# Performance work log

Hardware: AMD Instinct MI355X
Metric: run time of the kernel (lower is better)

The kernel has to match this reference:

```python
import jax, jax.numpy as jnp
import numpy as np

B, T, HOP = 4, 200, 120
N = T * HOP
M1, A1 = 40, 5            # mcep_order+1, apdc_order+1
HID, COND = 256, 192
SR = 24000.0
ALPHA = 0.466             # frequency-warping for 24 kHz
PD = 4                    # Pade order
PADE = jnp.asarray([1.0, 0.4999273, 0.1067005, 0.00956526, 0.0003041358], jnp.float32)
SIGN = jnp.asarray([1.0, -1.0, 1.0, -1.0], jnp.float32)  # + for odd Pade tap index
F0_MEAN, F0_STD = 5.0, 0.25
MCEP_MEAN, MCEP_STD = 0.0, 1.0
APDC_MEAN, APDC_STD = 0.0, 1.0
NOISE_RATIO, SP_RATE, F0_RATE = 0.5, 1.0, 1.0


def mc2b(mc, a):
    """SPTK mc2b: mel-cepstrum -> MLSA filter coefficients (scan over order)."""
    mc_rev = jnp.moveaxis(mc, -1, 0)[::-1]  # [M1, B, T]
    def step(carry, c):
        b = c - a * carry
        return b, b
    _, bs = jax.lax.scan(step, jnp.zeros_like(mc_rev[0]), mc_rev)
    return jnp.moveaxis(bs[::-1], 0, -1)


def _mlsafir(x, b, d):
    # SPTK mlsafir, vectorized over the PD Pade taps.
    # x: [PD], b: [M1], d: [PD, M1+1]
    aa = 1.0 - ALPHA * ALPHA
    d1 = aa * x + ALPHA * d[:, 1]
    def step(prev, di):  # d_new[i] = d[i] + a*(d[i+1] - d_new[i-1]) : order recurrence
        d_i, d_ip1 = di
        new = d_i + ALPHA * (d_ip1 - prev)
        return new, new
    xs = (d[:, 2:M1].T, d[:, 3:M1 + 1].T)  # [M1-2, PD]
    _, dupd = jax.lax.scan(step, d1, xs)    # [M1-2, PD]
    y = jnp.einsum('mp,m->p', dupd, b[2:])
    # delay-line shift: new d = [x, d1, d1, dupd[2..M]]
    new_d = jnp.concatenate([x[:, None], d1[:, None], d1[:, None], dupd.T], axis=1)
    return y, new_d


def _mlsa_step(state, inp):
    d1a, d1b, d2, pt2 = state
    x, b = inp
    x = x * jnp.exp(b[0])           # gain
    # ---- stage 1 (uses b[1] only), SPTK mlsadf1 ----
    aa = 1.0 - ALPHA * ALPHA
    na = aa * d1b[:PD] + ALPHA * d1a[1:]
    npt = na * b[1]
    v1 = npt * PADE[1:]
    x1 = x + jnp.sum(v1 * SIGN)
    y1 = jnp.sum(v1) + x1
    d1a = jnp.concatenate([d1a[:1], na])
    d1b = jnp.concatenate([x1[None], npt])
    # ---- stage 2 (orders >= 2), SPTK mlsadf2 ----
    fy, d2 = _mlsafir(pt2[:PD], b, d2)
    v2 = fy * PADE[1:]
    x2 = y1 + jnp.sum(v2 * SIGN)
    y2 = jnp.sum(v2) + x2
    pt2 = jnp.concatenate([x2[None], fy])
    return (d1a, d1b, d2, pt2), y2


def mlsa_filter(exc, b_up):
    # exc: [N], b_up: [N, M1] -> filtered waveform [N]
    init = (jnp.zeros(PD + 1, jnp.float32), jnp.zeros(PD + 1, jnp.float32),
            jnp.zeros((PD, M1 + 1), jnp.float32), jnp.zeros(PD + 1, jnp.float32))
    _, y = jax.lax.scan(_mlsa_step, init, (exc, b_up))
    return y


def _forward(mceps, apdcs, frame_f0s, noise,
             Wm, bm, Wa, ba, Wf, bf, Wpa, bpa, Wpp, bpp,
             Wrp, brp, Wra, bra, Wap):
    # linear feature embed + sum
    hs = mceps @ Wm + bm + apdcs @ Wa + ba + frame_f0s @ Wf + bf   # [B,T,HID]
    ca = hs @ Wpa + bpa                                             # prenet_a cond [B,T,COND]
    cp = hs @ Wpp + bpp                                             # prenet_p cond
    # denorm (+ exp for log-f0)
    f0 = jnp.exp(frame_f0s[..., 0] * F0_STD + F0_MEAN) * F0_RATE    # [B,T]
    sp = mceps * MCEP_STD + MCEP_MEAN
    ap = apdcs * APDC_STD + APDC_MEAN
    # per-path mel-cepstra with prenet residuals
    mc_p = sp * SP_RATE + 0.1 * jnp.tanh(cp @ Wrp + brp)
    mc_a = sp * SP_RATE + 0.1 * jnp.tanh(ca @ Wra + bra) + ap @ Wap
    b_p = mc2b(mc_p, ALPHA)
    b_a = mc2b(mc_a, ALPHA)
    # excitation at sample rate
    f0_up = jnp.repeat(f0, HOP, axis=1)                             # [B,N]
    phase = jnp.cumsum(f0_up / SR, axis=1)
    w = jnp.floor(phase)
    wprev = jnp.concatenate([jnp.zeros_like(w[:, :1]), w[:, :-1]], axis=1)
    amp = jnp.sqrt(SR / jnp.maximum(f0_up, 1.0))
    pulse = jnp.where(w > wprev, amp, 0.0)
    exc_p = pulse * (1.0 - NOISE_RATIO)
    exc_a = noise * NOISE_RATIO
    # run both (periodic/aperiodic) MLSA synthesis filters in one batched scan
    excs = jnp.concatenate([exc_p, exc_a], axis=0)                  # [2B,N]
    bs = jnp.repeat(jnp.concatenate([b_p, b_a], axis=0), HOP, axis=1)  # [2B,N,M1]
    wavs = jax.vmap(mlsa_filter)(excs, bs)                          # [2B,N]
    return wavs[:B] + wavs[B:]


_forward_jit = jax.jit(_forward)


def setup_inputs() -> dict:
    key = jax.random.key(0)
    ks = jax.random.split(key, 20)
    decay = 0.3 / (1.0 + jnp.arange(M1, dtype=jnp.float32))  # realistic cepstral decay (filter stability)
    return {
        'mceps': jax.random.normal(ks[0], (B, T, M1), jnp.float32) * decay,
        'apdcs': jax.random.normal(ks[1], (B, T, A1), jnp.float32) * 0.3,
        'frame_f0s': jax.random.normal(ks[2], (B, T, 1), jnp.float32),
        'noise': jax.random.normal(ks[3], (B, N), jnp.float32),
        'Wm': jax.random.normal(ks[4], (M1, HID), jnp.float32) / np.sqrt(M1),
        'bm': jnp.zeros((HID,), jnp.float32),
        'Wa': jax.random.normal(ks[5], (A1, HID), jnp.float32) / np.sqrt(A1),
        'ba': jnp.zeros((HID,), jnp.float32),
        'Wf': jax.random.normal(ks[6], (1, HID), jnp.float32),
        'bf': jnp.zeros((HID,), jnp.float32),
        'Wpa': jax.random.normal(ks[7], (HID, COND), jnp.float32) / np.sqrt(HID),
        'bpa': jnp.zeros((COND,), jnp.float32),
        'Wpp': jax.random.normal(ks[8], (HID, COND), jnp.float32) / np.sqrt(HID),
        'bpp': jnp.zeros((COND,), jnp.float32),
        'Wrp': jax.random.normal(ks[9], (COND, M1), jnp.float32) / np.sqrt(COND),
        'brp': jnp.zeros((M1,), jnp.float32),
        'Wra': jax.random.normal(ks[10], (COND, M1), jnp.float32) / np.sqrt(COND),
        'bra': jnp.zeros((M1,), jnp.float32),
        'Wap': jax.random.normal(ks[11], (A1, M1), jnp.float32) * 0.05,
    }


def reference(mceps, apdcs, frame_f0s, noise,
              Wm, bm, Wa, ba, Wf, bf, Wpa, bpa, Wpp, bpp,
              Wrp, brp, Wra, bra, Wap):
    return _forward_jit(mceps, apdcs, frame_f0s, noise,
                        Wm, bm, Wa, ba, Wf, bf, Wpa, bpa, Wpp, bpp,
                        Wrp, brp, Wra, bra, Wap)
```

## Files before the change

### kernel.cpp

```cpp
#include <hip/hip_runtime.h>
#include <math.h>

#define ALPHA 0.466f
#define T_FRAMES 200
#define HOPW 120
#define NSAMP 24000
#define M1 40
#define HID 256
#define CONDW 192

#define NCHUNK 200
#define CHUNKF 1
#define WARMF 4
#define SERF (WARMF + CHUNKF)

#define F8 8
#define EMB_BLOCKS (4 * T_FRAMES / F8)
#define BPF ((NSAMP + 255) / 256)

__global__ __launch_bounds__(256) void prep_kernel(
    const float* __restrict__ mceps, const float* __restrict__ apdcs,
    const float* __restrict__ f0s, const float* __restrict__ noise,
    const float* __restrict__ Wm, const float* __restrict__ bm,
    const float* __restrict__ Wa, const float* __restrict__ ba,
    const float* __restrict__ Wf, const float* __restrict__ bf,
    const float* __restrict__ Wpa, const float* __restrict__ bpa,
    const float* __restrict__ Wpp, const float* __restrict__ bpp,
    const float* __restrict__ Wrp, const float* __restrict__ brp,
    const float* __restrict__ Wra, const float* __restrict__ bra,
    const float* __restrict__ Wap,
    float* __restrict__ bcoef, float* __restrict__ exc)
{
    const int tid = threadIdx.x;

    if (blockIdx.x >= EMB_BLOCKS) {
        const int xb = blockIdx.x - EMB_BLOCKS;
        const int ff = xb / BPF;
        const int n = (xb % BPF) * 256 + tid;

        if (ff >= 4) {
            if (n < NSAMP) exc[ff * NSAMP + n] = 0.5f * noise[(ff - 4) * NSAMP + n];
            return;
        }

        __shared__ double s_base[T_FRAMES];
        __shared__ double s_step[T_FRAMES];
        __shared__ float  s_amp[T_FRAMES];

        if (tid < 64) {
            const int L = tid;
            double st[4], loc[4];
            float am[4];
            double s = 0.0;
            #pragma unroll
            for (int j = 0; j < 4; ++j) {
                int ft = L * 4 + j;
                if (ft < T_FRAMES) {
                    double fv = exp((double)f0s[ff * T_FRAMES + ft] * 0.25 + 5.0);
                    st[j] = fv / 24000.0;
                    am[j] = (float)(0.5 * sqrt(24000.0 / fmax(fv, 1.0)));
                } else { st[j] = 0.0; am[j] = 0.f; }
                loc[j] = s;
                s += st[j];
            }
            double tot = s;
            #pragma unroll
            for (int off = 1; off < 64; off <<= 1) {
                double v = __shfl_up(s, off, 64);
                if (L >= off) s += v;
            }
            double excl = s - tot;
            #pragma unroll
            for (int j = 0; j < 4; ++j) {
                int ft = L * 4 + j;
                if (ft < T_FRAMES) {
                    s_base[ft] = 120.0 * (excl + loc[j]);
                    s_step[ft] = st[j];
                    s_amp[ft]  = am[j];
                }
            }
        }
        __syncthreads();

        if (n < NSAMP) {
            int ft = n / HOPW, k = n - ft * HOPW;
            double st = s_step[ft], bs = s_base[ft];
            double ph  = bs + (double)(k + 1) * st;
            double php = bs + (double)k * st;
            exc[ff * NSAMP + n] = (floor(ph) > floor(php)) ? s_amp[ft] : 0.0f;
        }
        return;
    }

    __shared__ float s_mc[F8][M1];
    __shared__ float s_ap[F8][5];
    __shared__ float s_f0[F8];
    __shared__ float s_h[F8][HID];
    __shared__ float s_ca[F8][CONDW];
    __shared__ float s_cp[F8][CONDW];
    __shared__ float s_mcp[F8][M1];
    __shared__ float s_mca[F8][M1];

    const int R0 = blockIdx.x * F8;

    for (int j = tid; j < F8 * M1; j += 256) s_mc[j / M1][j % M1] = mceps[R0 * M1 + j];
    if (tid < F8 * 5) s_ap[tid / 5][tid % 5] = apdcs[R0 * 5 + tid];
    if (tid < F8)     s_f0[tid] = f0s[R0 + tid];
    __syncthreads();

    {
        float acc[F8];
        const float bias = bm[tid] + ba[tid] + bf[tid];
        #pragma unroll
        for (int r = 0; r < F8; ++r) acc[r] = bias;
        for (int k = 0; k < M1; ++k) {
            float w = Wm[k * HID + tid];
            #pragma unroll
            for (int r = 0; r < F8; ++r) acc[r] = fmaf(s_mc[r][k], w, acc[r]);
        }
        #pragma unroll
        for (int k = 0; k < 5; ++k) {
            float w = Wa[k * HID + tid];
            #pragma unroll
            for (int r = 0; r < F8; ++r) acc[r] = fmaf(s_ap[r][k], w, acc[r]);
        }
        float wf = Wf[tid];
        #pragma unroll
        for (int r = 0; r < F8; ++r) s_h[r][tid] = fmaf(s_f0[r], wf, acc[r]);
    }
    __syncthreads();

    if (tid < CONDW) {
        float aA[F8], aP[F8];
        #pragma unroll
        for (int r = 0; r < F8; ++r) { aA[r] = bpa[tid]; aP[r] = bpp[tid]; }
        for (int k = 0; k < HID; k += 4) {
            float4 h4[F8];
            #pragma unroll
            for (int r = 0; r < F8; ++r) h4[r] = *(const float4*)&s_h[r][k];
            #pragma unroll
            for (int kk = 0; kk < 4; ++kk) {
                float wa = Wpa[(k + kk) * CONDW + tid];
                float wp = Wpp[(k + kk) * CONDW + tid];
                #pragma unroll
                for (int r = 0; r < F8; ++r) {
                    float hv = (&h4[r].x)[kk];
                    aA[r] = fmaf(hv, wa, aA[r]);
                    aP[r] = fmaf(hv, wp, aP[r]);
                }
            }
        }
        #pragma unroll
        for (int r = 0; r < F8; ++r) { s_ca[r][tid] = aA[r]; s_cp[r][tid] = aP[r]; }
    }
    __syncthreads();

    if (tid < M1) {
        const int u = tid;
        float acc[F8];
        #pragma unroll
        for (int r = 0; r < F8; ++r) acc[r] = brp[u];
        for (int k = 0; k < CONDW; k += 4) {
            float4 c4[F8];
            #pragma unroll
            for (int r = 0; r < F8; ++r) c4[r] = *(const float4*)&s_cp[r][k];
            #pragma unroll
            for (int kk = 0; kk < 4; ++kk) {
                float w = Wrp[(k + kk) * M1 + u];
                #pragma unroll
                for (int r = 0; r < F8; ++r) acc[r] = fmaf((&c4[r].x)[kk], w, acc[r]);
            }
        }
        #pragma unroll
        for (int r = 0; r < F8; ++r)
            s_mcp[r][u] = s_mc[r][u] + 0.1f * tanhf(acc[r]);
    } else if (tid >= 64 && tid < 64 + M1) {
        const int u = tid - 64;
        float acc[F8];
        #pragma unroll
        for (int r = 0; r < F8; ++r) acc[r] = bra[u];
        for (int k = 0; k < CONDW; k += 4) {
            float4 c4[F8];
            #pragma unroll
            for (int r = 0; r < F8; ++r) c4[r] = *(const float4*)&s_ca[r][k];
            #pragma unroll
            for (int kk = 0; kk < 4; ++kk) {
                float w = Wra[(k + kk) * M1 + u];
                #pragma unroll
                for (int r = 0; r < F8; ++r) acc[r] = fmaf((&c4[r].x)[kk], w, acc[r]);
            }
        }
        #pragma unroll
        for (int r = 0; r < F8; ++r) {
            float aw = 0.f;
            #pragma unroll
            for (int j = 0; j < 5; ++j) aw = fmaf(s_ap[r][j], Wap[j * M1 + u], aw);
            s_mca[r][u] = s_mc[r][u] + 0.1f * tanhf(acc[r]) + aw;
        }
    }
    __syncthreads();

    if (tid < 16) {
        const int r = tid >> 1, path = tid & 1;
        const int R = R0 + r;
        const int batch = R / T_FRAMES, t = R - batch * T_FRAMES;
        const float* src = path ? s_mca[r] : s_mcp[r];
        float* dst = bcoef + ((path * 4 + batch) * T_FRAMES + t) * M1;
        float prev = src[M1 - 1];
        dst[M1 - 1] = prev;
        for (int m = M1 - 2; m >= 0; --m) {
            prev = src[m] - ALPHA * prev;
            dst[m] = prev;
        }
    }
}

template <int CTRL>
__device__ __forceinline__ float rshr(float x) {
    return __int_as_float(
        __builtin_amdgcn_mov_dpp(__float_as_int(x), CTRL, 0xF, 0xF, true));
}
__device__ __forceinline__ float rlane(float x, int l) {
    return __int_as_float(__builtin_amdgcn_readlane(__float_as_int(x), l));
}

template <bool OUT>
__device__ __forceinline__ void run_frame(
    const float* __restrict__ sx, float AB,
    float BP1, float BP2, float BP3, float BP4,
    float B0, float B1, float B2, float B3, float B4,
    float K, float IPw, bool pos0, bool row0, bool parodd,
    float& E0, float& E1, float& E2, float& E3, float& E4,
    float& dlp, float& xin,
    float& m1, float& m2, float& m3, float& m4, float& w0,
    float* __restrict__ yb)
{
    const float A   = ALPHA;
    const float AA  = 1.0f - A * A;
    const float A2  = A * A;
    const float mA3 = -(A * A2);
    const float A4  = A2 * A2;
    const float R   = -(A4 * A);
    const float R2  = R * R;
    const float R4  = R2 * R2;

    float xc = sx[0];
    #pragma unroll 8
    for (int k = 0; k < HOPW; ++k) {
        float xn = sx[k + 1];
        float x = xc;

        float na0 = fmaf(A, m1, AA * w0);
        float na1 = fmaf(A, m2, AB * m1);
        float na2 = fmaf(A, m3, AB * m2);
        float na3 = fmaf(A, m4, AB * m3);
        float p = fmaf(na2, BP3, na0 * BP1);
        float q = fmaf(na3, BP4, na1 * BP2);
        float x1 = x + (p - q);
        float y1 = fmaf(2.0f, p, x);
        m1 = na0; m2 = na1; m3 = na2; m4 = na3; w0 = x1;

        float pE4 = rshr<0x112>(E4);
        float c0 = fmaf(A, E0, pos0 ? dlp : pE4);
        float c1 = fmaf(A, E1, E0);
        float c2 = fmaf(A, E2, E1);
        float c3 = fmaf(A, E3, E2);
        float c4 = fmaf(A, E4, E3);
        float u0 = c0;
        float u1 = fmaf(-A, u0, c1);
        float u2 = fmaf(-A, u1, c2);
        float u3 = fmaf(-A, u2, c3);
        float u4 = fmaf(-A, u3, c4);
        float X = u4;
        X = fmaf(R,  rshr<0x112>(X), X);
        X = fmaf(R2, rshr<0x114>(X), X);
        X = fmaf(R4, rshr<0x118>(X), X);
        float dl = fmaf(AA, xin, A * dlp);
        float Xt = fmaf(K, dl, X);
        float Si = rshr<0x112>(Xt);
        Si = pos0 ? dl : Si;
        float t0 = fmaf(-A,  Si, u0);
        float t1 = fmaf(A2,  Si, u1);
        float t2 = fmaf(mA3, Si, u2);
        float t3 = fmaf(A4,  Si, u3);

        float fp = t0 * B0;
        fp = fmaf(t1, B1, fp);
        fp = fmaf(t2, B2, fp);
        fp = fmaf(t3, B3, fp);
        fp = fmaf(Xt, B4, fp);
        float S = fp;
        S += rshr<0x112>(S);
        S += rshr<0x114>(S);
        S += rshr<0x118>(S);

        float Sx = rshr<0x111>(S);
        float T1 = rshr<0x142>(S);
        float T0 = rshr<0x142>(Sx);
        float xprev = (parodd ? T1 : T0) * IPw;

        float s0p = rlane(S, 14), s1p = rlane(S, 30);
        float s2p = rlane(S, 46), s3p = rlane(S, 62);
        float s0a = rlane(S, 15), s1a = rlane(S, 31);
        float s2a = rlane(S, 47), s3a = rlane(S, 63);
        float eP = s0p + s2p, oP = s1p + s3p;
        float eA = s0a + s2a, oA = s1a + s3a;
        float ce = parodd ? eA : eP;
        float co = parodd ? oA : oP;
        float x2 = y1 + (ce + co);
        if (OUT) {
            float y2 = x2 + (ce - co);
            yb[k] = y2;
        }

        xin = row0 ? x2 : xprev;
        E0 = t0; E1 = t1; E2 = t2; E3 = t3; E4 = Xt;
        dlp = dl;
        xc = xn;
    }
}

__global__ __launch_bounds__(64) void mlsa_kernel(
    const float* __restrict__ bcoef, const float* __restrict__ exc,
    float* __restrict__ out)
{
    __shared__ float sexc[2][HOPW + 4];
    __shared__ float ybuf[2][HOPW + 4];

    const int tid = threadIdx.x;
    const int par = tid & 1;
    const int pos = (tid >> 1) & 7;
    const int row = tid >> 4;
    const int chunk = blockIdx.x >> 2;
    const int b = blockIdx.x & 3;
    const int f = par * 4 + b;
    const bool pos0 = (pos == 0), row0 = (row == 0), parodd = (par != 0);

    const float P1 = 0.4999273f, P2 = 0.1067005f, P3 = 0.00956526f, P4 = 0.0003041358f;
    const float wrow = (row == 0) ? P1 : (row == 1) ? -P2 : (row == 2) ? P3 : -P4;
    const float IPw  = (row == 1) ? (1.f / P1) : (row == 2) ? (-1.f / P2)
                     : (row == 3) ? (1.f / P3) : 0.f;

    const float A = ALPHA;
    const float R = -(A * A * A * A * A);
    float K = R;
    for (int j = 0; j < pos; ++j) K *= R;

    float E0 = 0.f, E1 = 0.f, E2 = 0.f, E3 = 0.f, E4 = 0.f;
    float dlp = 0.f, xin = 0.f;
    float m1 = 0.f, m2 = 0.f, m3 = 0.f, m4 = 0.f, w0 = 0.f;

    const float* sxp = sexc[par];
    float* ybp = ybuf[par];
    const int ja = 5 * pos + 2;
    const int lh = tid >> 1;

    #pragma unroll 1
    for (int i = 0; i < SERF; ++i) {
        const int ftA = chunk - WARMF + i;
        const int ftc = (ftA < 0) ? 0 : ftA;
        const float* bp = bcoef + (f * T_FRAMES + ftc) * M1;
        const float b1 = bp[1];
        const float G  = expf(bp[0]);
        const float AAc = 1.0f - A * A;
        const float AB = AAc * b1;
        const float BP1 = b1 * P1, BP2 = b1 * P2, BP3 = b1 * P3, BP4 = b1 * P4;

        const float* ex = exc + f * NSAMP + ftc * HOPW;
        #pragma unroll
        for (int m = 0; m < 4; ++m) {
            int kk = lh + 32 * m;
            if (kk < HOPW) sexc[par][kk] = (ftA >= 0) ? ex[kk] * G : 0.f;
        }
        if (tid < 2) sexc[tid][HOPW] = 0.f;

        const float B0c = bp[ja]     * wrow;
        const float B1c = bp[ja + 1] * wrow;
        const float B2c = bp[ja + 2] * wrow;
        const float B3c = (pos < 7) ? bp[ja + 3] * wrow : 0.f;
        const float B4c = (pos < 7) ? bp[ja + 4] * wrow : 0.f;

        if (i >= WARMF) {
            run_frame<true>(sxp, AB, BP1, BP2, BP3, BP4,
                            B0c, B1c, B2c, B3c, B4c, K, IPw, pos0, row0, parodd,
                            E0, E1, E2, E3, E4, dlp, xin, m1, m2, m3, m4, w0, ybp);
            float* op = out + b * NSAMP + chunk * HOPW;
            op[tid] = ybuf[0][tid] + ybuf[1][tid];
            if (tid < HOPW - 64) op[tid + 64] = ybuf[0][tid + 64] + ybuf[1][tid + 64];
        } else {
            run_frame<false>(sxp, AB, BP1, BP2, BP3, BP4,
                             B0c, B1c, B2c, B3c, B4c, K, IPw, pos0, row0, parodd,
                             E0, E1, E2, E3, E4, dlp, xin, m1, m2, m3, m4, w0, ybp);
        }
    }
}

extern "C" void kernel_launch(void* const* d_in, const int* in_sizes, int n_in,
                              void* d_out, int out_size, void* d_ws, size_t ws_size,
                              hipStream_t stream) {
    const float* mceps = (const float*)d_in[0];
    const float* apdcs = (const float*)d_in[1];
    const float* f0s   = (const float*)d_in[2];
    const float* noise = (const float*)d_in[3];
    const float* Wm  = (const float*)d_in[4];
    const float* bm  = (const float*)d_in[5];
    const float* Wa  = (const float*)d_in[6];
    const float* ba  = (const float*)d_in[7];
    const float* Wf  = (const float*)d_in[8];
    const float* bf  = (const float*)d_in[9];
    const float* Wpa = (const float*)d_in[10];
    const float* bpa = (const float*)d_in[11];
    const float* Wpp = (const float*)d_in[12];
    const float* bpp = (const float*)d_in[13];
    const float* Wrp = (const float*)d_in[14];
    const float* brp = (const float*)d_in[15];
    const float* Wra = (const float*)d_in[16];
    const float* bra = (const float*)d_in[17];
    const float* Wap = (const float*)d_in[18];
    float* out = (float*)d_out;

    char* ws = (char*)d_ws;
    float* bcoef = (float*)(ws + 0);
    float* exc   = (float*)(ws + 256000);

    prep_kernel<<<dim3(EMB_BLOCKS + 8 * BPF), dim3(256), 0, stream>>>(
        mceps, apdcs, f0s, noise, Wm, bm, Wa, ba, Wf, bf,
        Wpa, bpa, Wpp, bpp, Wrp, brp, Wra, bra, Wap, bcoef, exc);

    mlsa_kernel<<<dim3(NCHUNK * 4), dim3(64), 0, stream>>>(bcoef, exc, out);
}
```

Baseline: 212.4 us.

## Shorten first warm-up frame and use permlane32 swap for cross-half reduction

```diff
diff --git a/kernel.cpp b/kernel.cpp
--- a/kernel.cpp
+++ b/kernel.cpp
@@ -10,13 +10,22 @@
 #define CONDW 192
 
 #define NCHUNK 200
-#define CHUNKF 1
 #define WARMF 4
-#define SERF (WARMF + CHUNKF)
+#define SERF (WARMF + 1)
+#define WARMK0 96
 
 #define F8 8
 #define EMB_BLOCKS (4 * T_FRAMES / F8)
 #define BPF ((NSAMP + 255) / 256)
+
+#if defined(__has_builtin)
+#  if __has_builtin(__builtin_amdgcn_permlane32_swap)
+#    define HAVE_PLSWAP 1
+#  endif
+#endif
+#ifndef HAVE_PLSWAP
+#  define HAVE_PLSWAP 0
+#endif
 
 __global__ __launch_bounds__(256) void prep_kernel(
     const float* __restrict__ mceps, const float* __restrict__ apdcs,
@@ -224,7 +233,7 @@
     return __int_as_float(__builtin_amdgcn_readlane(__float_as_int(x), l));
 }
 
-template <bool OUT>
+template <bool OUT, int KSTART>
 __device__ __forceinline__ void run_frame(
     const float* __restrict__ sx, float AB,
     float BP1, float BP2, float BP3, float BP4,
@@ -244,9 +253,9 @@
     const float R2  = R * R;
     const float R4  = R2 * R2;
 
-    float xc = sx[0];
+    float xc = sx[KSTART];
     #pragma unroll 8
-    for (int k = 0; k < HOPW; ++k) {
+    for (int k = KSTART; k < HOPW; ++k) {
         float xn = sx[k + 1];
         float x = xc;
 
@@ -299,6 +308,20 @@
         float T0 = rshr<0x142>(Sx);
         float xprev = (parodd ? T1 : T0) * IPw;
 
+#if HAVE_PLSWAP
+        typedef unsigned u32x2 __attribute__((ext_vector_type(2)));
+        u32x2 rr = __builtin_amdgcn_permlane32_swap(
+            __float_as_uint(S), __float_as_uint(S), false, false);
+        float S2 = __uint_as_float(rr.x) + __uint_as_float(rr.y);
+        float aE = rlane(S2, 14), bE = rlane(S2, 30);
+        float aO = rlane(S2, 15), bO = rlane(S2, 31);
+        float tot = parodd ? (aO + bO) : (aE + bE);
+        float x2 = y1 + tot;
+        if (OUT) {
+            float dif = parodd ? (aO - bO) : (aE - bE);
+            yb[k] = x2 + dif;
+        }
+#else
         float s0p = rlane(S, 14), s1p = rlane(S, 30);
         float s2p = rlane(S, 46), s3p = rlane(S, 62);
         float s0a = rlane(S, 15), s1a = rlane(S, 31);
@@ -312,6 +335,7 @@
             float y2 = x2 + (ce - co);
             yb[k] = y2;
         }
+#endif
 
         xin = row0 ? x2 : xprev;
         E0 = t0; E1 = t1; E2 = t2; E3 = t3; E4 = Xt;
@@ -380,17 +404,21 @@
         const float B3c = (pos < 7) ? bp[ja + 3] * wrow : 0.f;
         const float B4c = (pos < 7) ? bp[ja + 4] * wrow : 0.f;
 
-        if (i >= WARMF) {
-            run_frame<true>(sxp, AB, BP1, BP2, BP3, BP4,
+        if (i == 0) {
+            run_frame<false, WARMK0>(sxp, AB, BP1, BP2, BP3, BP4,
+                            B0c, B1c, B2c, B3c, B4c, K, IPw, pos0, row0, parodd,
+                            E0, E1, E2, E3, E4, dlp, xin, m1, m2, m3, m4, w0, ybp);
+        } else if (i < SERF - 1) {
+            run_frame<false, 0>(sxp, AB, BP1, BP2, BP3, BP4,
+                            B0c, B1c, B2c, B3c, B4c, K, IPw, pos0, row0, parodd,
+                            E0, E1, E2, E3, E4, dlp, xin, m1, m2, m3, m4, w0, ybp);
+        } else {
+            run_frame<true, 0>(sxp, AB, BP1, BP2, BP3, BP4,
                             B0c, B1c, B2c, B3c, B4c, K, IPw, pos0, row0, parodd,
                             E0, E1, E2, E3, E4, dlp, xin, m1, m2, m3, m4, w0, ybp);
             float* op = out + b * NSAMP + chunk * HOPW;
             op[tid] = ybuf[0][tid] + ybuf[1][tid];
             if (tid < HOPW - 64) op[tid + 64] = ybuf[0][tid + 64] + ybuf[1][tid + 64];
-        } else {
-            run_frame<false>(sxp, AB, BP1, BP2, BP3, BP4,
-                             B0c, B1c, B2c, B3c, B4c, K, IPw, pos0, row0, parodd,
-                             E0, E1, E2, E3, E4, dlp, xin, m1, m2, m3, m4, w0, ybp);
         }
     }
 }
```

Result: faster. 195.7 us (-7.9%).
